# Kernel optimization log

Measured on AMD Instinct MI355X. Metric: run time of the kernel, lower is better.

The kernel has to match this reference:

```python
import jax, jax.numpy as jnp
import numpy as np

B, L, DM = 4, 2048, 1024  # batch, seq len (== l_max, global kernel), d_model; head_dim = 1


def setup_inputs() -> dict:
    key = jax.random.key(0)
    ks = jax.random.split(key, 13)
    n = lambda k, shape, s=1.0: jax.random.normal(k, shape, dtype=jnp.float32) * s
    W_SCALE = 0.02   # keeps activations well-conditioned through the chained convs
    K_SCALE = 0.02
    return {
        "u": n(ks[0], (B, L, DM)),
        "Wq": n(ks[1], (DM, DM), W_SCALE), "bq": n(ks[2], (DM,), W_SCALE),
        "Wk": n(ks[3], (DM, DM), W_SCALE), "bk": n(ks[4], (DM,), W_SCALE),
        "Wv": n(ks[5], (DM, DM), W_SCALE), "bv": n(ks[6], (DM,), W_SCALE),
        "k_kernel": n(ks[7], (DM, L), K_SCALE),
        "k_D": n(ks[8], (DM,)),
        "ssm_kernel": n(ks[9], (DM, L), K_SCALE),
        "D": n(ks[10], (DM,)),
        "Wo": n(ks[11], (DM, DM), W_SCALE), "bo": n(ks[12], (DM,), W_SCALE),
    }


def reference(u, Wq, bq, Wk, bk, Wv, bv, k_kernel, k_D, ssm_kernel, D, Wo, bo):
    # u: (B, L, H) with H = d_model (head_dim = 1)
    Lseq = u.shape[1]
    fft_size = 2 * Lseq  # zero-pad to 2L for linear (causal) convolution

    # q/k/v projections -> (B, H, L)
    q = jnp.einsum('blh,dh->bdl', u, Wq) + bq[None, :, None]
    k = jnp.einsum('blh,dh->bdl', u, Wk) + bk[None, :, None]
    v = jnp.einsum('blh,dh->bdl', u, Wv) + bv[None, :, None]

    # shift conv on k: k <- k_kernel * k (causal FFT conv) + k_D * k
    k_kernel_f = jnp.fft.rfft(k_kernel, n=fft_size)           # (H, F)
    k_f = jnp.fft.rfft(k, n=fft_size)                          # (B, H, F)
    shift_k = jnp.fft.irfft(k_kernel_f[None] * k_f, n=fft_size)[..., :Lseq]
    k = shift_k + k_D[None, :, None] * k

    # head_dim == 1: kv outer product collapses to elementwise gate
    kv = k * v                                                 # (B, H, L)

    # ssm conv on kv (torch's 1/fft_size + norm='forward' irfft == standard irfft)
    kv_f = jnp.fft.rfft(kv, n=fft_size)                        # (B, H, F)
    ssm_kernel_f = jnp.fft.rfft(ssm_kernel, n=fft_size)        # (H, F)
    y = jnp.fft.irfft(kv_f * ssm_kernel_f[None], n=fft_size)[..., :Lseq]
    y = y + kv * D[None, :, None]                              # D skip

    # q gating, then output projection
    y = y * q                                                  # (B, H, L)
    y = jnp.swapaxes(y, 1, 2)                                  # (B, L, H)
    return jnp.einsum('blh,oh->blo', y, Wo) + bo
```

## Files before the change

kernel.cpp:

```cpp
#include <hip/hip_runtime.h>
#include <hip/hip_bf16.h>
#include <stdint.h>

#define DM   1024
#define LSEQ 2048
#define NB   4

typedef __attribute__((ext_vector_type(8))) short  short8;
typedef __attribute__((ext_vector_type(4))) float  floatx4;

__device__ __forceinline__ ushort f2b(float x) {
    union { float f; uint32_t u; } v; v.f = x;
    uint32_t b = v.u + 0x7FFF + ((v.u >> 16) & 1);
    return (ushort)(b >> 16);
}
__device__ __forceinline__ float b2f(ushort x) {
    union { uint32_t u; float f; } v; v.u = ((uint32_t)x) << 16;
    return v.f;
}

__global__ __launch_bounds__(256) void cvt_bf16_kernel(const float* __restrict__ in,
                                                       ushort* __restrict__ out, int n8) {
    int i = blockIdx.x * 256 + threadIdx.x;
    if (i >= n8) return;
    const float4* p = (const float4*)in + (size_t)i * 2;
    float4 a = p[0], b = p[1];
    union { ushort us[8]; uint4 v; } o;
    o.us[0] = f2b(a.x); o.us[1] = f2b(a.y); o.us[2] = f2b(a.z); o.us[3] = f2b(a.w);
    o.us[4] = f2b(b.x); o.us[5] = f2b(b.y); o.us[6] = f2b(b.z); o.us[7] = f2b(b.w);
    ((uint4*)out)[i] = o.v;
}

__global__ __launch_bounds__(256) void cvt_w_kernel(const float* __restrict__ Wq,
                                                    const float* __restrict__ Wk,
                                                    const float* __restrict__ Wv,
                                                    const float* __restrict__ Wo,
                                                    ushort* __restrict__ dst) {
    const int per = DM * DM / 8;
    int i = blockIdx.x * 256 + threadIdx.x;
    int r = i / per;
    const float* src = (r == 0) ? Wq : (r == 1) ? Wk : (r == 2) ? Wv : Wo;
    int j = i - r * per;
    const float4* p = (const float4*)src + (size_t)j * 2;
    float4 a = p[0], b = p[1];
    union { ushort us[8]; uint4 v; } o;
    o.us[0] = f2b(a.x); o.us[1] = f2b(a.y); o.us[2] = f2b(a.z); o.us[3] = f2b(a.w);
    o.us[4] = f2b(b.x); o.us[5] = f2b(b.y); o.us[6] = f2b(b.z); o.us[7] = f2b(b.w);
    ((uint4*)dst)[i] = o.v;
}

template <int MODE>
__global__ __launch_bounds__(256) void gemm_bt(const ushort* __restrict__ Aw,
                                               const ushort* __restrict__ Bw,
                                               const float* __restrict__ b0,
                                               const float* __restrict__ b1,
                                               const float* __restrict__ b2,
                                               void* __restrict__ C0v,
                                               void* __restrict__ C1v,
                                               void* __restrict__ C2v,
                                               int M, int N, int K, int nbx) {
    constexpr int BM = 128, BN = 128, BK = 32;
    __shared__ ushort As[BM * BK];
    __shared__ ushort Bs[BN * BK];

    const int tid   = threadIdx.x;
    const int wave  = tid >> 6;
    const int lane  = tid & 63;
    const int qlane = lane & 15;
    const int qk    = lane >> 4;

    int flat = blockIdx.y * nbx + blockIdx.x;
    int nwg  = nbx * gridDim.y;
    int swz  = (flat & 7) * (nwg >> 3) + (flat >> 3);
    const int tn = (swz % nbx) * BN;
    const int tm = (swz / nbx) * BM;

    const int wm = (wave >> 1) * 64;
    const int wn = (wave & 1) * 64;

    floatx4 acc[4][4] = {};

    for (int k0 = 0; k0 < K; k0 += BK) {
        __syncthreads();
#pragma unroll
        for (int j = 0; j < 2; ++j) {
            int chunk = tid + j * 256;
            int row   = chunk >> 2;
            int col   = (chunk & 3) * 8;
            const ushort* gpA = Aw + (size_t)(tm + row) * K + k0 + col;
            const ushort* gpB = Bw + (size_t)(tn + row) * K + k0 + col;
            int base = (j * 256 + wave * 64) * 16;
            __builtin_amdgcn_global_load_lds((const __attribute__((address_space(1))) void*)gpA,
                                             (__attribute__((address_space(3))) void*)((char*)As + base),
                                             16, 0, 0);
            __builtin_amdgcn_global_load_lds((const __attribute__((address_space(1))) void*)gpB,
                                             (__attribute__((address_space(3))) void*)((char*)Bs + base),
                                             16, 0, 0);
        }
        __syncthreads();

        short8 af[4], bfv[4];
#pragma unroll
        for (int i = 0; i < 4; ++i)
            af[i] = *(const short8*)(As + (wm + i * 16 + qlane) * BK + qk * 8);
#pragma unroll
        for (int j = 0; j < 4; ++j)
            bfv[j] = *(const short8*)(Bs + (wn + j * 16 + qlane) * BK + qk * 8);
#pragma unroll
        for (int i = 0; i < 4; ++i)
#pragma unroll
            for (int j = 0; j < 4; ++j)
                acc[i][j] = __builtin_amdgcn_mfma_f32_16x16x32_bf16(af[i], bfv[j], acc[i][j], 0, 0, 0);
    }

#pragma unroll
    for (int i = 0; i < 4; ++i) {
#pragma unroll
        for (int j = 0; j < 4; ++j) {
            int n  = tn + wn + j * 16 + qlane;
            int m0 = tm + wm + i * 16 + qk * 4;
            if (MODE == 0) {
                int proj = n >> 10, dd = n & (DM - 1);
                const float* bb = (proj == 0) ? b0 : (proj == 1) ? b1 : b2;
                ushort* Cb      = (ushort*)((proj == 0) ? C0v : (proj == 1) ? C1v : C2v);
                float bv = bb[dd];
                int b = m0 >> 11, l = m0 & (LSEQ - 1);
                ushort4 val;
                val.x = f2b(acc[i][j][0] + bv);
                val.y = f2b(acc[i][j][1] + bv);
                val.z = f2b(acc[i][j][2] + bv);
                val.w = f2b(acc[i][j][3] + bv);
                *(ushort4*)(Cb + ((size_t)b * DM + dd) * LSEQ + l) = val;
            } else {
                float* C0 = (float*)C0v;
                float bv = b0[n];
#pragma unroll
                for (int r = 0; r < 4; ++r)
                    C0[(size_t)(m0 + r) * N + n] = acc[i][j][r] + bv;
            }
        }
    }
}

#define KSTR 2096
#define XSTR 2248

__global__ __launch_bounds__(512) void conv_mfma_kernel(const ushort* __restrict__ x,
                                                        const float* __restrict__ ker,
                                                        const float* __restrict__ scale,
                                                        const ushort* __restrict__ gate,
                                                        ushort* __restrict__ out) {
    __shared__ ushort krev[KSTR];
    __shared__ ushort xs[4 * XSTR];
    const int d    = blockIdx.x;
    const int tid  = threadIdx.x;
    const int wave = tid >> 6;
    const int lane = tid & 63;

    {
        int b = wave >> 1, half = wave & 1;
        const ushort* src = x + ((size_t)b * DM + d) * LSEQ + half * 1024 + lane * 8;
        char* dst = (char*)xs + b * (XSTR * 2) + 256 + half * 2048;
#pragma unroll
        for (int c = 0; c < 2; ++c)
            __builtin_amdgcn_global_load_lds((const __attribute__((address_space(1))) void*)(src + c * 512),
                                             (__attribute__((address_space(3))) void*)(dst + c * 1024),
                                             16, 0, 0);
    }
    {
        const float* krow = ker + (size_t)d * LSEQ;
        int e0 = tid * 4;
        float4 kv = *(const float4*)(krow + e0);
        ushort4 o;
        o.x = f2b(kv.w); o.y = f2b(kv.z); o.z = f2b(kv.y); o.w = f2b(kv.x);
        *(ushort4*)(krev + (2060 - e0)) = o;
        uint4 z = {0, 0, 0, 0};
        if (tid < 2)  *(uint4*)((char*)krev + tid * 16) = z;
        if (tid >= 2 && tid < 6) *(uint4*)((char*)krev + 4128 + (tid - 2) * 16) = z;
        if (tid >= 64 && tid < 128) {
            int b = (tid - 64) >> 4, c = (tid - 64) & 15;
            *(uint4*)((char*)xs + b * (XSTR * 2) + c * 16) = z;
        }
        if (tid >= 128 && tid < 144) {
            int b = (tid - 128) >> 2, c = (tid - 128) & 3;
            *(uint4*)((char*)xs + b * (XSTR * 2) + 4352 + c * 16) = z;
        }
    }
    __syncthreads();

    const int qn = lane & 15;
    const int qk = lane >> 4;

    int g[2] = {wave, 15 - wave};
    const int smax_all = 128 * (15 - wave) + 128;

    const int lbase = (qn & 3) * XSTR + 128 + 16 * (qn >> 2) + 8 * qk;

    floatx4 acc[2][2] = {};

    short8 fE[2], fO[2];
#pragma unroll
    for (int gi = 0; gi < 2; ++gi) {
        fE[gi] = *(const short8*)(xs + lbase + 128 * g[gi] + 64);
        fO[gi] = *(const short8*)(xs + lbase + 128 * g[gi] + 32);
    }

#define CSTEP(SS, FP)                                                                        \
    {                                                                                        \
        int b_el = 2063 - qn + 8 * qk - (SS);                                                \
        int A0 = b_el & ~3;                                                                  \
        uint2 w0 = *(const uint2*)(krev + A0);                                               \
        uint2 w1 = *(const uint2*)(krev + A0 + 4);                                           \
        uint2 w2 = *(const uint2*)(krev + A0 + 8);                                           \
        int qsel = (b_el >> 1) & 1;                                                          \
        uint sh  = (uint)(b_el & 1) * 16u;                                                   \
        uint e0 = qsel ? w0.y : w0.x;                                                        \
        uint e1 = qsel ? w1.x : w0.y;                                                        \
        uint e2 = qsel ? w1.y : w1.x;                                                        \
        uint e3 = qsel ? w2.x : w1.y;                                                        \
        uint e4 = qsel ? w2.y : w2.x;                                                        \
        union { uint u[4]; short8 v; } Af;                                                   \
        Af.u[0] = __builtin_amdgcn_alignbit(e1, e0, sh);                                     \
        Af.u[1] = __builtin_amdgcn_alignbit(e2, e1, sh);                                     \
        Af.u[2] = __builtin_amdgcn_alignbit(e3, e2, sh);                                     \
        Af.u[3] = __builtin_amdgcn_alignbit(e4, e3, sh);                                     \
        _Pragma("unroll")                                                                    \
        for (int gi = 0; gi < 2; ++gi) {                                                     \
            if ((SS) <= 128 * g[gi] + 128) {                                                 \
                short8 fN = *(const short8*)(xs + lbase + 128 * g[gi] - (SS));               \
                acc[gi][0] = __builtin_amdgcn_mfma_f32_16x16x32_bf16(Af.v, fN, acc[gi][0], 0, 0, 0); \
                acc[gi][1] = __builtin_amdgcn_mfma_f32_16x16x32_bf16(Af.v, FP[gi], acc[gi][1], 0, 0, 0); \
                FP[gi] = fN;                                                                 \
            }                                                                                \
        }                                                                                    \
    }

    for (int s = 0; s <= smax_all; s += 64) {
        CSTEP(s, fE);
        if (s + 32 <= smax_all) CSTEP(s + 32, fO);
    }
#undef CSTEP

    const float sc = scale[d];
#pragma unroll
    for (int gi = 0; gi < 2; ++gi) {
#pragma unroll
        for (int m = 0; m < 2; ++m) {
            int p  = 8 * g[gi] + 4 * m + (qn >> 2);
            int b  = qn & 3;
            int l0 = 16 * p + 4 * qk;
            size_t off = ((size_t)b * DM + d) * LSEQ + l0;
            ushort4 xv = *(const ushort4*)(xs + b * XSTR + 128 + l0);
            ushort4 gv = *(const ushort4*)(gate + off);
            ushort4 ov;
            ov.x = f2b((acc[gi][m][0] + sc * b2f(xv.x)) * b2f(gv.x));
            ov.y = f2b((acc[gi][m][1] + sc * b2f(xv.y)) * b2f(gv.y));
            ov.z = f2b((acc[gi][m][2] + sc * b2f(xv.z)) * b2f(gv.z));
            ov.w = f2b((acc[gi][m][3] + sc * b2f(xv.w)) * b2f(gv.w));
            *(ushort4*)(out + off) = ov;
        }
    }
}

__global__ __launch_bounds__(256) void transpose_bf16(const ushort* __restrict__ in,
                                                      ushort* __restrict__ out) {
    __shared__ ushort t[32][36];
    const int l0 = blockIdx.x * 32;
    const int d0 = blockIdx.y * 32;
    const int b  = blockIdx.z;
    const int q  = threadIdx.x & 7;
    const int r  = threadIdx.x >> 3;
    *(ushort4*)(&t[r][q * 4]) = *(const ushort4*)(in + ((size_t)b * DM + d0 + r) * LSEQ + l0 + q * 4);
    __syncthreads();
    ushort4 o;
    o.x = t[q * 4 + 0][r]; o.y = t[q * 4 + 1][r]; o.z = t[q * 4 + 2][r]; o.w = t[q * 4 + 3][r];
    *(ushort4*)(out + ((size_t)b * LSEQ + l0 + r) * DM + d0 + q * 4) = o;
}

extern "C" void kernel_launch(void* const* d_in, const int* in_sizes, int n_in,
                              void* d_out, int out_size, void* d_ws, size_t ws_size,
                              hipStream_t stream) {
    const float* u        = (const float*)d_in[0];
    const float* Wq       = (const float*)d_in[1];
    const float* bq       = (const float*)d_in[2];
    const float* Wk       = (const float*)d_in[3];
    const float* bk       = (const float*)d_in[4];
    const float* Wv       = (const float*)d_in[5];
    const float* bv       = (const float*)d_in[6];
    const float* k_kernel = (const float*)d_in[7];
    const float* k_D      = (const float*)d_in[8];
    const float* ssm_ker  = (const float*)d_in[9];
    const float* Dv       = (const float*)d_in[10];
    const float* Wo       = (const float*)d_in[11];
    const float* bo       = (const float*)d_in[12];
    float* outp = (float*)d_out;

    char* ws = (char*)d_ws;
    ushort* Q    = (ushort*)(ws);
    ushort* KV   = (ushort*)(ws + (16ull << 20));
    ushort* V    = (ushort*)(ws + (32ull << 20));
    ushort* U16  = (ushort*)(ws + (48ull << 20));
    ushort* YT   = (ushort*)(ws + (64ull << 20));
    ushort* Wcat = (ushort*)(ws + (80ull << 20));

    cvt_bf16_kernel<<<(NB * LSEQ * DM / 8) / 256, 256, 0, stream>>>(u, U16, NB * LSEQ * DM / 8);
    cvt_w_kernel<<<(4 * DM * DM / 8) / 256, 256, 0, stream>>>(Wq, Wk, Wv, Wo, Wcat);

    dim3 g1(3 * DM / 128, NB * LSEQ / 128);
    gemm_bt<0><<<g1, 256, 0, stream>>>(U16, Wcat, bq, bk, bv, Q, KV, V,
                                       NB * LSEQ, 3 * DM, DM, 3 * DM / 128);

    conv_mfma_kernel<<<DM, 512, 0, stream>>>(KV, k_kernel, k_D, V, KV);
    conv_mfma_kernel<<<DM, 512, 0, stream>>>(KV, ssm_ker, Dv, Q, KV);

    dim3 g2(LSEQ / 32, DM / 32, NB);
    transpose_bf16<<<g2, 256, 0, stream>>>(KV, YT);

    dim3 g3(DM / 128, NB * LSEQ / 128);
    gemm_bt<1><<<g3, 256, 0, stream>>>(YT, Wcat + 3 * DM * DM, bo, bo, bo,
                                       outp, outp, outp, NB * LSEQ, DM, DM, DM / 128);
}
```

Baseline: 185.7 us.

## Rewrite bf16 GEMM with 3-stage LDS pipeline, swizzled layout and larger tiles

Replaces the single-buffered 128x128x32 GEMM with a 512-thread 128x256x64 variant. It prefetches two K-tiles ahead into a triple-buffered LDS ring, waiting on vmcnt instead of doing a full sync each iteration. An XOR swizzle on the LDS slots avoids bank conflicts, and setprio raises priority around the MFMA bursts. The aim is to hide global-load latency and raise MFMA utilisation in both projection GEMMs. The cost is 144KB of LDS per block, which lowers occupancy, and grid sizes that shrink to fewer workgroups.

```diff
diff --git a/kernel.cpp b/kernel.cpp
--- a/kernel.cpp
+++ b/kernel.cpp
@@ -50,18 +50,18 @@
 }
 
 template <int MODE>
-__global__ __launch_bounds__(256) void gemm_bt(const ushort* __restrict__ Aw,
-                                               const ushort* __restrict__ Bw,
-                                               const float* __restrict__ b0,
-                                               const float* __restrict__ b1,
-                                               const float* __restrict__ b2,
-                                               void* __restrict__ C0v,
-                                               void* __restrict__ C1v,
-                                               void* __restrict__ C2v,
-                                               int M, int N, int K, int nbx) {
-    constexpr int BM = 128, BN = 128, BK = 32;
-    __shared__ ushort As[BM * BK];
-    __shared__ ushort Bs[BN * BK];
+__global__ __launch_bounds__(512, 2) void gemm_bt2(const ushort* __restrict__ Aw,
+                                                   const ushort* __restrict__ Bw,
+                                                   const float* __restrict__ b0,
+                                                   const float* __restrict__ b1,
+                                                   const float* __restrict__ b2,
+                                                   void* __restrict__ C0v,
+                                                   void* __restrict__ C1v,
+                                                   void* __restrict__ C2v,
+                                                   int M, int N, int K, int nbx) {
+    constexpr int BM = 128, BN = 256, BK = 64;
+    constexpr int BUFB = 49152;
+    __shared__ char lds[3 * BUFB];
 
     const int tid   = threadIdx.x;
     const int wave  = tid >> 6;
@@ -75,50 +75,82 @@
     const int tn = (swz % nbx) * BN;
     const int tm = (swz / nbx) * BM;
 
-    const int wm = (wave >> 1) * 64;
-    const int wn = (wave & 1) * 64;
+    const int wmo = (wave >> 2) * 64;
+    const int wno = (wave & 3) * 64;
+    const int NT  = K / BK;
+
+#define STAGE(kt, p)                                                                          \
+    {                                                                                         \
+        const int k0_ = (kt) * BK;                                                            \
+        char* Ab_ = lds + (p) * BUFB;                                                         \
+        char* Bb_ = Ab_ + 16384;                                                              \
+        _Pragma("unroll")                                                                     \
+        for (int j = 0; j < 2; ++j) {                                                         \
+            int id = wave * 64 + lane + j * 512;                                              \
+            int row = id >> 3, s = id & 7;                                                    \
+            const ushort* src = Aw + (size_t)(tm + row) * K + k0_ + ((s ^ (row & 7)) * 8);    \
+            __builtin_amdgcn_global_load_lds((const __attribute__((address_space(1))) void*)src, \
+                (__attribute__((address_space(3))) void*)(Ab_ + wave * 1024 + j * 8192), 16, 0, 0); \
+        }                                                                                     \
+        _Pragma("unroll")                                                                     \
+        for (int j = 0; j < 4; ++j) {                                                         \
+            int id = wave * 64 + lane + j * 512;                                              \
+            int row = id >> 3, s = id & 7;                                                    \
+            const ushort* src = Bw + (size_t)(tn + row) * K + k0_ + ((s ^ (row & 7)) * 8);    \
+            __builtin_amdgcn_global_load_lds((const __attribute__((address_space(1))) void*)src, \
+                (__attribute__((address_space(3))) void*)(Bb_ + wave * 1024 + j * 8192), 16, 0, 0); \
+        }                                                                                     \
+    }
 
     floatx4 acc[4][4] = {};
 
-    for (int k0 = 0; k0 < K; k0 += BK) {
-        __syncthreads();
-#pragma unroll
-        for (int j = 0; j < 2; ++j) {
-            int chunk = tid + j * 256;
-            int row   = chunk >> 2;
-            int col   = (chunk & 3) * 8;
-            const ushort* gpA = Aw + (size_t)(tm + row) * K + k0 + col;
-            const ushort* gpB = Bw + (size_t)(tn + row) * K + k0 + col;
-            int base = (j * 256 + wave * 64) * 16;
-            __builtin_amdgcn_global_load_lds((const __attribute__((address_space(1))) void*)gpA,
-                                             (__attribute__((address_space(3))) void*)((char*)As + base),
-                                             16, 0, 0);
-            __builtin_amdgcn_global_load_lds((const __attribute__((address_space(1))) void*)gpB,
-                                             (__attribute__((address_space(3))) void*)((char*)Bs + base),
-                                             16, 0, 0);
-        }
-        __syncthreads();
-
-        short8 af[4], bfv[4];
-#pragma unroll
-        for (int i = 0; i < 4; ++i)
-            af[i] = *(const short8*)(As + (wm + i * 16 + qlane) * BK + qk * 8);
-#pragma unroll
-        for (int j = 0; j < 4; ++j)
-            bfv[j] = *(const short8*)(Bs + (wn + j * 16 + qlane) * BK + qk * 8);
-#pragma unroll
-        for (int i = 0; i < 4; ++i)
-#pragma unroll
-            for (int j = 0; j < 4; ++j)
-                acc[i][j] = __builtin_amdgcn_mfma_f32_16x16x32_bf16(af[i], bfv[j], acc[i][j], 0, 0, 0);
-    }
+    STAGE(0, 0);
+    STAGE(1, 1);
+
+    const int z7 = qlane & 7;
+
+    for (int t = 0; t < NT; ++t) {
+        const int cur = t % 3;
+        if (t < NT - 1) asm volatile("s_waitcnt vmcnt(6)" ::: "memory");
+        else            asm volatile("s_waitcnt vmcnt(0)" ::: "memory");
+        __builtin_amdgcn_s_barrier();
+        __builtin_amdgcn_sched_barrier(0);
+
+        if (t + 2 < NT) STAGE(t + 2, (t + 2) % 3);
+
+        const char* Ab = lds + cur * BUFB;
+        const char* Bb = Ab + 16384;
+#pragma unroll
+        for (int kk = 0; kk < 2; ++kk) {
+            const int slot = ((kk * 4 + qk) ^ z7) << 4;
+            short8 af[4], bfv[4];
+#pragma unroll
+            for (int i = 0; i < 4; ++i) {
+                int r = wmo + i * 16 + qlane;
+                af[i] = *(const short8*)(Ab + r * 128 + slot);
+            }
+#pragma unroll
+            for (int j = 0; j < 4; ++j) {
+                int r = wno + j * 16 + qlane;
+                bfv[j] = *(const short8*)(Bb + r * 128 + slot);
+            }
+            __builtin_amdgcn_s_setprio(1);
+#pragma unroll
+            for (int i = 0; i < 4; ++i)
+#pragma unroll
+                for (int j = 0; j < 4; ++j)
+                    acc[i][j] = __builtin_amdgcn_mfma_f32_16x16x32_bf16(af[i], bfv[j], acc[i][j], 0, 0, 0);
+            __builtin_amdgcn_s_setprio(0);
+        }
+    }
+#undef STAGE
 
 #pragma unroll
     for (int i = 0; i < 4; ++i) {
 #pragma unroll
         for (int j = 0; j < 4; ++j) {
-            int n  = tn + wn + j * 16 + qlane;
-            int m0 = tm + wm + i * 16 + qk * 4;
+            int n  = tn + wno + j * 16 + qlane;
+            int m0 = tm + wmo + i * 16 + qk * 4;
             if (MODE == 0) {
                 int proj = n >> 10, dd = n & (DM - 1);
                 const float* bb = (proj == 0) ? b0 : (proj == 1) ? b1 : b2;
@@ -306,9 +338,9 @@
     cvt_bf16_kernel<<<(NB * LSEQ * DM / 8) / 256, 256, 0, stream>>>(u, U16, NB * LSEQ * DM / 8);
     cvt_w_kernel<<<(4 * DM * DM / 8) / 256, 256, 0, stream>>>(Wq, Wk, Wv, Wo, Wcat);
 
-    dim3 g1(3 * DM / 128, NB * LSEQ / 128);
-    gemm_bt<0><<<g1, 256, 0, stream>>>(U16, Wcat, bq, bk, bv, Q, KV, V,
-                                       NB * LSEQ, 3 * DM, DM, 3 * DM / 128);
+    dim3 g1(3 * DM / 256, NB * LSEQ / 128);
+    gemm_bt2<0><<<g1, 512, 0, stream>>>(U16, Wcat, bq, bk, bv, Q, KV, V,
+                                        NB * LSEQ, 3 * DM, DM, 3 * DM / 256);
 
     conv_mfma_kernel<<<DM, 512, 0, stream>>>(KV, k_kernel, k_D, V, KV);
     conv_mfma_kernel<<<DM, 512, 0, stream>>>(KV, ssm_ker, Dv, Q, KV);
@@ -316,7 +348,7 @@
     dim3 g2(LSEQ / 32, DM / 32, NB);
     transpose_bf16<<<g2, 256, 0, stream>>>(KV, YT);
 
-    dim3 g3(DM / 128, NB * LSEQ / 128);
-    gemm_bt<1><<<g3, 256, 0, stream>>>(YT, Wcat + 3 * DM * DM, bo, bo, bo,
-                                       outp, outp, outp, NB * LSEQ, DM, DM, DM / 128);
-}
+    dim3 g3(DM / 256, NB * LSEQ / 128);
+    gemm_bt2<1><<<g3, 512, 0, stream>>>(YT, Wcat + 3 * DM * DM, bo, bo, bo,
+                                        outp, outp, outp, NB * LSEQ, DM, DM, DM / 256);
+}
```

Result: faster. 172.2 us (-7.3%).
